# Performance work log

Measured on AMD Instinct MI355X. Metric: run time of the kernel, lower is better.

The kernel has to match this reference:

```python
import jax, jax.numpy as jnp
import numpy as np


def swiglu(g, u):
    return jax.nn.silu(g) * u


def setup_inputs() -> dict:
    key = jax.random.key(0)
    ks = jax.random.split(key, 10)
    D, H, E, HS = 2048, 512, 32, 1024
    B, S = 1, 2048
    s = 0.02
    return {
        "x": jax.random.normal(ks[0], (B, S, D), jnp.float32),
        "gate_w": jax.random.normal(ks[1], (E, D), jnp.float32) * s,
        "expert_bias": jnp.zeros((E,), jnp.float32),
        "wg": jax.random.normal(ks[2], (E, D, H), jnp.float32) * s,
        "wu": jax.random.normal(ks[3], (E, D, H), jnp.float32) * s,
        "wd": jax.random.normal(ks[4], (E, H, D), jnp.float32) * s,
        "sg": jax.random.normal(ks[5], (D, HS), jnp.float32) * s,
        "su": jax.random.normal(ks[6], (D, HS), jnp.float32) * s,
        "sd": jax.random.normal(ks[7], (HS, D), jnp.float32) * s,
        "coef_w": jax.random.normal(ks[8], (2, D), jnp.float32) * s,
        "coef_b": jnp.zeros((2,), jnp.float32),
        "top_k": 4,
    }


def reference(x, gate_w, expert_bias, wg, wu, wd, sg, su, sd, coef_w, coef_b, top_k):
    # --- sigmoid router with bias-adjusted top-k selection ---
    logits = jnp.einsum("bsd,ed->bse", x, gate_w)            # [B,S,E]
    routing = jax.nn.sigmoid(logits.astype(jnp.float32))
    biased = routing + expert_bias[None, None, :]
    _, inds = jax.lax.top_k(biased, top_k)                    # [B,S,k]
    scores = jnp.take_along_axis(routing, inds, axis=-1)      # gather UNbiased weights
    scores = scores / (jnp.sum(scores, axis=-1, keepdims=True) + 1e-20)  # norm_topk_prob
    scores = scores.astype(x.dtype)

    # --- SwitchGLU experts: dense per-expert SwiGLU, then gather top-k outputs ---
    h = jnp.einsum("bsd,edh->bseh", x, wg)                    # [B,S,E,H]
    u = jnp.einsum("bsd,edh->bseh", x, wu)
    y_all = jnp.einsum("bseh,ehd->bsed", swiglu(h, u), wd)    # [B,S,E,D]
    expert_out = jnp.take_along_axis(
        y_all, inds[..., None], axis=2)                        # [B,S,k,D]
    y_experts = jnp.sum(expert_out * scores[..., None], axis=-2)  # [B,S,D]

    # --- shared expert + learned 2-way mixing coefficient ---
    shared = swiglu(x @ sg, x @ su) @ sd                      # [B,S,D]
    coef = jax.nn.softmax(jnp.einsum("bsd,cd->bsc", x, coef_w) + coef_b, axis=-1)
    return y_experts * coef[..., :1] + shared * coef[..., 1:]
```

## Files before the change

### kernel.cpp

```cpp
#include <hip/hip_runtime.h>
#include <hip/hip_bf16.h>
#include <stdint.h>

#define S_TOK   2048
#define DMODEL  2048
#define HEXP    512
#define NEXP    32
#define HSH     1024
#define NPAIR   (S_TOK * 4)
#define NT128   96

#define M128_NT  0
#define M128_TE  1
#define M128_TP0 (1 + NT128)
#define M128_TM  (1 + 2 * NT128)
#define META_SIZE (1 + 3 * NT128)

typedef short  s16x8 __attribute__((ext_vector_type(8)));
typedef __bf16 b16x8 __attribute__((ext_vector_type(8)));
typedef float  f32x4 __attribute__((ext_vector_type(4)));

__device__ __forceinline__ f32x4 mfma16x16x32(s16x8 a, s16x8 b, f32x4 c) {
    return __builtin_amdgcn_mfma_f32_16x16x32_bf16(
        __builtin_bit_cast(b16x8, a), __builtin_bit_cast(b16x8, b), c, 0, 0, 0);
}

__device__ __forceinline__ unsigned short f2bf(float f) {
    union { float f; unsigned int u; } v; v.f = f;
    unsigned int u = v.u;
    return (unsigned short)((u + 0x7FFFu + ((u >> 16) & 1u)) >> 16);
}

__device__ __forceinline__ float bf2f(unsigned short b) {
    union { unsigned int u; float f; } v; v.u = ((unsigned int)b) << 16;
    return v.f;
}

__device__ __forceinline__ void gload16(const unsigned short* g, unsigned short* l) {
    __builtin_amdgcn_global_load_lds(
        (const __attribute__((address_space(1))) void*)(uintptr_t)g,
        (__attribute__((address_space(3))) void*)(uintptr_t)l, 16, 0, 0);
}

__device__ __forceinline__ int src_col8(int lane) {
    return 8 * ((lane & 3) ^ ((lane >> 3) & 3));
}
__device__ __forceinline__ int frag_ko(int fr, int fq) {
    return 8 * (fq ^ ((fr >> 1) & 3));
}

__device__ __forceinline__ void tconv_tile(const float* __restrict__ s,
                                           unsigned short* __restrict__ d,
                                           const int K, const int N,
                                           const int k0, const int n0,
                                           unsigned short* pool)
{
    auto T = (unsigned short (*)[84])pool;
    const int tid = threadIdx.x;
    const int n4 = (tid & 15) * 4;
    const int kr = tid >> 4;
#pragma unroll
    for (int i = 0; i < 4; ++i) {
        const int k = kr + i * 16;
        const float4 v = *reinterpret_cast<const float4*>(s + (size_t)(k0 + k) * N + n0 + n4);
        T[n4 + 0][k] = f2bf(v.x);
        T[n4 + 1][k] = f2bf(v.y);
        T[n4 + 2][k] = f2bf(v.z);
        T[n4 + 3][k] = f2bf(v.w);
    }
    __syncthreads();
    const int nw = tid >> 2;
    const int kc = (tid & 3) * 16;
    const uint2 a0 = *reinterpret_cast<const uint2*>(&T[nw][kc]);
    const uint2 a1 = *reinterpret_cast<const uint2*>(&T[nw][kc + 4]);
    const uint2 a2 = *reinterpret_cast<const uint2*>(&T[nw][kc + 8]);
    const uint2 a3 = *reinterpret_cast<const uint2*>(&T[nw][kc + 12]);
    uint4 w0, w1;
    w0.x = a0.x; w0.y = a0.y; w0.z = a1.x; w0.w = a1.y;
    w1.x = a2.x; w1.y = a2.y; w1.z = a3.x; w1.w = a3.y;
    unsigned short* o = d + (size_t)(n0 + nw) * K + k0 + kc;
    *reinterpret_cast<uint4*>(o)     = w0;
    *reinterpret_cast<uint4*>(o + 8) = w1;
}

__global__ __launch_bounds__(256)
void router_kernel(const float* __restrict__ x, const float* __restrict__ gate_w,
                   const float* __restrict__ expert_bias,
                   const float* __restrict__ coef_w, const float* __restrict__ coef_b,
                   int* __restrict__ inds, float* __restrict__ scores,
                   float* __restrict__ coefo)
{
    const int t = blockIdx.x;
    const int tid = threadIdx.x;
    const int lane = tid & 63;
    const int wave = tid >> 6;
    const float* xr = x + (size_t)t * DMODEL;

    float xv[32];
#pragma unroll
    for (int j = 0; j < 32; ++j) xv[j] = xr[lane + 64 * j];

    __shared__ float s_logits[NEXP];
    __shared__ float s_coef[2];

    for (int i = 0; i < 8; ++i) {
        const int e = wave * 8 + i;
        const float* wr = gate_w + (size_t)e * DMODEL;
        float p = 0.f;
#pragma unroll
        for (int j = 0; j < 32; ++j) p += xv[j] * wr[lane + 64 * j];
#pragma unroll
        for (int o = 32; o > 0; o >>= 1) p += __shfl_xor(p, o);
        if (lane == 0) s_logits[e] = p;
    }
    if (wave == 0) {
        for (int c = 0; c < 2; ++c) {
            const float* wr = coef_w + (size_t)c * DMODEL;
            float p = 0.f;
#pragma unroll
            for (int j = 0; j < 32; ++j) p += xv[j] * wr[lane + 64 * j];
#pragma unroll
            for (int o = 32; o > 0; o >>= 1) p += __shfl_xor(p, o);
            if (lane == 0) s_coef[c] = p;
        }
    }
    __syncthreads();
    if (tid == 0) {
        float routing[NEXP], biased[NEXP];
        for (int e = 0; e < NEXP; ++e) {
            const float r = 1.f / (1.f + expf(-s_logits[e]));
            routing[e] = r;
            biased[e] = r + expert_bias[e];
        }
        int sel[4]; float sc[4]; float ssum = 0.f;
        for (int k = 0; k < 4; ++k) {
            int best = 0; float bv = -1e30f;
            for (int e = 0; e < NEXP; ++e)
                if (biased[e] > bv) { bv = biased[e]; best = e; }
            sel[k] = best; sc[k] = routing[best]; ssum += sc[k];
            biased[best] = -1e30f;
        }
        const float inv = 1.f / (ssum + 1e-20f);
        for (int k = 0; k < 4; ++k) {
            inds[t * 4 + k] = sel[k];
            scores[t * 4 + k] = sc[k] * inv;
        }
        const float l0 = s_coef[0] + coef_b[0];
        const float l1 = s_coef[1] + coef_b[1];
        const float m = fmaxf(l0, l1);
        const float e0 = expf(l0 - m), e1 = expf(l1 - m);
        coefo[t * 2 + 0] = e0 / (e0 + e1);
        coefo[t * 2 + 1] = e1 / (e0 + e1);
    }
}

__global__ __launch_bounds__(256)
void xcast_kernel(const float* __restrict__ x, unsigned short* __restrict__ xb)
{
    const int i = (blockIdx.x * 256 + threadIdx.x) * 4;
    const float4 v = *reinterpret_cast<const float4*>(x + i);
    ushort4 o;
    o.x = f2bf(v.x); o.y = f2bf(v.y); o.z = f2bf(v.z); o.w = f2bf(v.w);
    *reinterpret_cast<ushort4*>(xb + i) = o;
}

__global__ __launch_bounds__(256)
void tconv_all_kernel(const float* __restrict__ wg, const float* __restrict__ wu,
                      const float* __restrict__ sg, const float* __restrict__ su,
                      unsigned short* __restrict__ W1, unsigned short* __restrict__ W2,
                      unsigned short* __restrict__ sgb, unsigned short* __restrict__ sub_)
{
    __shared__ unsigned short pool[64 * 84];
    const int bid = blockIdx.x;
    if (bid < 8192) {
        const int e = bid >> 8, t = bid & 255;
        tconv_tile(wg + (size_t)e * DMODEL * HEXP, W1 + (size_t)e * HEXP * DMODEL,
                   DMODEL, HEXP, ((t >> 3) & 31) * 64, (t & 7) * 64, pool);
    } else if (bid < 16384) {
        const int e = (bid - 8192) >> 8, t = bid & 255;
        tconv_tile(wu + (size_t)e * DMODEL * HEXP, W2 + (size_t)e * HEXP * DMODEL,
                   DMODEL, HEXP, ((t >> 3) & 31) * 64, (t & 7) * 64, pool);
    } else if (bid < 16896) {
        const int t = bid - 16384;
        tconv_tile(sg, sgb, DMODEL, HSH, (t >> 4) * 64, (t & 15) * 64, pool);
    } else {
        const int t = bid - 16896;
        tconv_tile(su, sub_, DMODEL, HSH, (t >> 4) * 64, (t & 15) * 64, pool);
    }
}

__global__ __launch_bounds__(1024)
void group_kernel(const int* __restrict__ inds, const float* __restrict__ scores,
                  int* __restrict__ meta, int* __restrict__ pair_token,
                  float* __restrict__ pair_score, int* __restrict__ tok_pos)
{
    __shared__ int cnt[NEXP];
    __shared__ int off_s[NEXP];
    __shared__ int cur[NEXP];
    const int tid = threadIdx.x;
    if (tid < NEXP) cnt[tid] = 0;
    __syncthreads();
    for (int i = tid; i < NPAIR; i += 1024) atomicAdd(&cnt[inds[i]], 1);
    __syncthreads();
    if (tid == 0) {
        int run = 0, nt1 = 0;
        for (int e = 0; e < NEXP; ++e) {
            off_s[e] = run;
            const int c = cnt[e];
            for (int m0 = 0; m0 < c; m0 += 128) {
                meta[M128_TE + nt1] = e;
                meta[M128_TP0 + nt1] = run + m0;
                meta[M128_TM + nt1] = (c - m0 < 128) ? (c - m0) : 128;
                ++nt1;
            }
            run += c;
        }
        meta[M128_NT] = nt1;
    }
    __syncthreads();
    if (tid < NEXP) cur[tid] = off_s[tid];
    __syncthreads();
    for (int i = tid; i < NPAIR; i += 1024) {
        const int e = inds[i];
        const int pos = atomicAdd(&cur[e], 1);
        pair_token[pos] = i >> 2;
        pair_score[pos] = scores[i];
        tok_pos[i] = pos;
    }
}

__global__ __launch_bounds__(256, 3)
void gu128_kernel(const unsigned short* __restrict__ xb,
                  const unsigned short* __restrict__ W1,
                  const unsigned short* __restrict__ W2,
                  const int* __restrict__ meta, const int* __restrict__ pair_token,
                  const unsigned short* __restrict__ sgb,
                  const unsigned short* __restrict__ sub_,
                  unsigned short* __restrict__ hexp, unsigned short* __restrict__ uexp,
                  unsigned short* __restrict__ shh, unsigned short* __restrict__ shu,
                  const float* __restrict__ wd, unsigned short* __restrict__ wdb,
                  const float* __restrict__ sd, unsigned short* __restrict__ sdb)
{
    constexpr int NT = DMODEL / 32;
    __shared__ unsigned short pool[16384];
    auto Al = (unsigned short (*)[128][32])(pool);
    auto Bl = (unsigned short (*)[128][32])(pool + 8192);

    const int bid = blockIdx.x;
    const int tid = threadIdx.x;
    const int lane = tid & 63;
    const int wave = tid >> 6;

    if (bid >= 8 * NT128 + 256) {
        const int idx = bid - (8 * NT128 + 256);
        if (idx < 8192) {
            const int e = idx >> 8, t = idx & 255;
            tconv_tile(wd + (size_t)e * HEXP * DMODEL, wdb + (size_t)e * DMODEL * HEXP,
                       HEXP, DMODEL, (t >> 5) * 64, (t & 31) * 64, pool);
        } else {
            const int t = idx - 8192;
            tconv_tile(sd, sdb, HSH, DMODEL, (t >> 5) * 64, (t & 31) * 64, pool);
        }
        return;
    }

    const int fr = lane & 15, fq = lane >> 4;
    const int ko = frag_ko(fr, fq);
    const int sub = lane >> 2;
    const int col8 = src_col8(lane);
    const int wm = wave >> 1, wn = wave & 1;
    const f32x4 zero4 = {0.f, 0.f, 0.f, 0.f};

    const bool EXPERT = bid < 8 * NT128;
    int p0, mval, n0, NB;
    const unsigned short* B;
    unsigned short* obuf;
    int tok0, tok1;
    const int arow0 = wave * 32 + sub;
    if (EXPERT) {
        const int tt = bid >> 3;
        if (tt >= meta[M128_NT]) return;
        const int e = meta[M128_TE + tt];
        p0 = meta[M128_TP0 + tt];
        mval = meta[M128_TM + tt];
        const int r = bid & 7;
        const int mat = r >> 2;
        n0 = (r & 3) * 128;
        NB = HEXP;
        B = (mat ? W2 : W1) + (size_t)e * HEXP * DMODEL;
        obuf = mat ? uexp : hexp;
        int q0 = p0 + arow0;      if (q0 > NPAIR - 1) q0 = NPAIR - 1;
        int q1 = p0 + arow0 + 16; if (q1 > NPAIR - 1) q1 = NPAIR - 1;
        tok0 = pair_token[q0];
        tok1 = pair_token[q1];
    } else {
        const int idx = bid - 8 * NT128;
        const int mat = idx & 1;
        n0 = ((idx >> 1) & 7) * 128;
        p0 = (idx >> 4) * 128;
        mval = 128;
        NB = HSH;
        B = mat ? sub_ : sgb;
        obuf = mat ? shu : shh;
        tok0 = p0 + arow0;
        tok1 = p0 + arow0 + 16;
    }

    const unsigned short* asrc0 = xb + (size_t)tok0 * DMODEL + col8;
    const unsigned short* asrc1 = xb + (size_t)tok1 * DMODEL + col8;
    const unsigned short* bsrc0 = B + (size_t)(n0 + arow0) * DMODEL + col8;
    const unsigned short* bsrc1 = B + (size_t)(n0 + arow0 + 16) * DMODEL + col8;

    auto stage = [&](int buf, int k0) {
        gload16(asrc0 + k0, &Al[buf][wave * 32][0]);
        gload16(asrc1 + k0, &Al[buf][wave * 32 + 16][0]);
        gload16(bsrc0 + k0, &Bl[buf][wave * 32][0]);
        gload16(bsrc1 + k0, &Bl[buf][wave * 32 + 16][0]);
    };

    f32x4 acc[4][4];
#pragma unroll
    for (int m = 0; m < 4; ++m)
#pragma unroll
        for (int n = 0; n < 4; ++n) acc[m][n] = zero4;

    auto compute = [&](int buf) {
        s16x8 af[4], bf[4];
#pragma unroll
        for (int m = 0; m < 4; ++m)
            af[m] = *reinterpret_cast<const s16x8*>(&Al[buf][wm * 64 + m * 16 + fr][ko]);
#pragma unroll
        for (int n = 0; n < 4; ++n)
            bf[n] = *reinterpret_cast<const s16x8*>(&Bl[buf][wn * 64 + n * 16 + fr][ko]);
#pragma unroll
        for (int m = 0; m < 4; ++m)
#pragma unroll
            for (int n = 0; n < 4; ++n)
                acc[m][n] = mfma16x16x32(af[m], bf[n], acc[m][n]);
    };

    stage(0, 0);
    __syncthreads();
#pragma unroll 1
    for (int t = 0; t < NT; ++t) {
        const int cur = t & 1;
        if (t + 1 < NT) stage(cur ^ 1, (t + 1) * 32);
        compute(cur);
        __syncthreads();
    }

#pragma unroll
    for (int m = 0; m < 4; ++m)
#pragma unroll
        for (int n = 0; n < 4; ++n) {
            const int col = n0 + wn * 64 + n * 16 + fr;
#pragma unroll
            for (int r = 0; r < 4; ++r) {
                const int rt = wm * 64 + m * 16 + fq * 4 + r;
                if (rt < mval)
                    obuf[(size_t)(p0 + rt) * NB + col] = f2bf(acc[m][n][r]);
            }
        }
}

__global__ __launch_bounds__(256)
void swiglu_kernel(const unsigned short* __restrict__ hexp,
                   const unsigned short* __restrict__ uexp,
                   unsigned short* __restrict__ act,
                   const unsigned short* __restrict__ shh,
                   const unsigned short* __restrict__ shu,
                   unsigned short* __restrict__ shact)
{
    constexpr size_t NE = (size_t)NPAIR * HEXP;
    const size_t i = ((size_t)blockIdx.x * 256 + threadIdx.x) * 8;
    const unsigned short *hp, *up;
    unsigned short* ap;
    size_t j;
    if (i < NE) { hp = hexp; up = uexp; ap = act; j = i; }
    else        { hp = shh;  up = shu;  ap = shact; j = i - NE; }
    const uint4 hv = *reinterpret_cast<const uint4*>(hp + j);
    const uint4 uv = *reinterpret_cast<const uint4*>(up + j);
    const unsigned short* hu = reinterpret_cast<const unsigned short*>(&hv);
    const unsigned short* uu = reinterpret_cast<const unsigned short*>(&uv);
    ushort4 o[2];
    unsigned short* ou = reinterpret_cast<unsigned short*>(o);
#pragma unroll
    for (int k = 0; k < 8; ++k) {
        const float h = bf2f(hu[k]);
        const float u = bf2f(uu[k]);
        ou[k] = f2bf(h / (1.f + __expf(-h)) * u);
    }
    *reinterpret_cast<uint4*>(ap + j) = *reinterpret_cast<const uint4*>(o);
}

__global__ __launch_bounds__(256, 3)
void down128_kernel(const unsigned short* __restrict__ act,
                    const unsigned short* __restrict__ shact,
                    const unsigned short* __restrict__ wdb,
                    const unsigned short* __restrict__ sdb,
                    unsigned short* __restrict__ ypair,
                    float* __restrict__ sdown,
                    const int* __restrict__ meta,
                    const float* __restrict__ pair_score)
{
    __shared__ unsigned short Al[2][128][32];
    __shared__ unsigned short Bl[2][128][32];

    const int bid = blockIdx.x;
    const int tid = threadIdx.x;
    const int lane = tid & 63;
    const int wave = tid >> 6;
    const int fr = lane & 15, fq = lane >> 4;
    const int ko = frag_ko(fr, fq);
    const int sub = lane >> 2;
    const int col8 = src_col8(lane);
    const int wm = wave >> 1, wn = wave & 1;
    const f32x4 zero4 = {0.f, 0.f, 0.f, 0.f};

    const bool EXPERT = bid < 16 * NT128;
    int p0, mval, n0, KA;
    const unsigned short *Asrc, *B;
    if (EXPERT) {
        const int tt = bid >> 4;
        if (tt >= meta[M128_NT]) return;
        const int e = meta[M128_TE + tt];
        p0 = meta[M128_TP0 + tt];
        mval = meta[M128_TM + tt];
        n0 = (bid & 15) * 128;
        KA = HEXP;
        Asrc = act;
        B = wdb + (size_t)e * DMODEL * HEXP;
    } else {
        const int idx = bid - 16 * NT128;
        p0 = (idx >> 4) * 128;
        mval = 128;
        n0 = (idx & 15) * 128;
        KA = HSH;
        Asrc = shact;
        B = sdb;
    }
    const int NT = KA / 32;

    const int arow0 = wave * 32 + sub;
    const unsigned short* asrc0 = Asrc + (size_t)(p0 + arow0) * KA + col8;
    const unsigned short* asrc1 = Asrc + (size_t)(p0 + arow0 + 16) * KA + col8;
    const unsigned short* bsrc0 = B + (size_t)(n0 + arow0) * KA + col8;
    const unsigned short* bsrc1 = B + (size_t)(n0 + arow0 + 16) * KA + col8;

    auto stage = [&](int buf, int k0) {
        gload16(asrc0 + k0, &Al[buf][wave * 32][0]);
        gload16(asrc1 + k0, &Al[buf][wave * 32 + 16][0]);
        gload16(bsrc0 + k0, &Bl[buf][wave * 32][0]);
        gload16(bsrc1 + k0, &Bl[buf][wave * 32 + 16][0]);
    };

    f32x4 acc[4][4];
#pragma unroll
    for (int m = 0; m < 4; ++m)
#pragma unroll
        for (int n = 0; n < 4; ++n) acc[m][n] = zero4;

    auto compute = [&](int buf) {
        s16x8 af[4], bf[4];
#pragma unroll
        for (int m = 0; m < 4; ++m)
            af[m] = *reinterpret_cast<const s16x8*>(&Al[buf][wm * 64 + m * 16 + fr][ko]);
#pragma unroll
        for (int n = 0; n < 4; ++n)
            bf[n] = *reinterpret_cast<const s16x8*>(&Bl[buf][wn * 64 + n * 16 + fr][ko]);
#pragma unroll
        for (int m = 0; m < 4; ++m)
#pragma unroll
            for (int n = 0; n < 4; ++n)
                acc[m][n] = mfma16x16x32(af[m], bf[n], acc[m][n]);
    };

    stage(0, 0);
    __syncthreads();
#pragma unroll 1
    for (int t = 0; t < NT; ++t) {
        const int cur = t & 1;
        if (t + 1 < NT) stage(cur ^ 1, (t + 1) * 32);
        compute(cur);
        __syncthreads();
    }

#pragma unroll
    for (int m = 0; m < 4; ++m)
#pragma unroll
        for (int n = 0; n < 4; ++n) {
            const int col = n0 + wn * 64 + n * 16 + fr;
#pragma unroll
            for (int r = 0; r < 4; ++r) {
                const int rt = wm * 64 + m * 16 + fq * 4 + r;
                if (rt < mval) {
                    if (EXPERT) {
                        const int p = p0 + rt;
                        ypair[(size_t)p * DMODEL + col] = f2bf(acc[m][n][r] * pair_score[p]);
                    } else {
                        sdown[(size_t)(p0 + rt) * DMODEL + col] = acc[m][n][r];
                    }
                }
            }
        }
}

__global__ __launch_bounds__(256)
void final_kernel(const unsigned short* __restrict__ ypair,
                  const float* __restrict__ sdown,
                  const float* __restrict__ coef, const int* __restrict__ tok_pos,
                  float* __restrict__ out)
{
    const int row = blockIdx.x;
    const int col = threadIdx.x * 8;
    float acc[8] = {0.f, 0.f, 0.f, 0.f, 0.f, 0.f, 0.f, 0.f};
#pragma unroll
    for (int k = 0; k < 4; ++k) {
        const int pos = tok_pos[row * 4 + k];
        const uint4 v = *reinterpret_cast<const uint4*>(ypair + (size_t)pos * DMODEL + col);
        const unsigned short* u = reinterpret_cast<const unsigned short*>(&v);
#pragma unroll
        for (int j = 0; j < 8; ++j) acc[j] += bf2f(u[j]);
    }
    const float c0 = coef[row * 2 + 0];
    const float c1 = coef[row * 2 + 1];
    const float* sd = sdown + (size_t)row * DMODEL + col;
    const float4 s0 = *reinterpret_cast<const float4*>(sd);
    const float4 s1 = *reinterpret_cast<const float4*>(sd + 4);
    float4 o0, o1;
    o0.x = acc[0] * c0 + s0.x * c1; o0.y = acc[1] * c0 + s0.y * c1;
    o0.z = acc[2] * c0 + s0.z * c1; o0.w = acc[3] * c0 + s0.w * c1;
    o1.x = acc[4] * c0 + s1.x * c1; o1.y = acc[5] * c0 + s1.y * c1;
    o1.z = acc[6] * c0 + s1.z * c1; o1.w = acc[7] * c0 + s1.w * c1;
    float* op = out + (size_t)row * DMODEL + col;
    *reinterpret_cast<float4*>(op) = o0;
    *reinterpret_cast<float4*>(op + 4) = o1;
}

extern "C" void kernel_launch(void* const* d_in, const int* in_sizes, int n_in,
                              void* d_out, int out_size, void* d_ws, size_t ws_size,
                              hipStream_t stream)
{
    const float* x           = (const float*)d_in[0];
    const float* gate_w      = (const float*)d_in[1];
    const float* expert_bias = (const float*)d_in[2];
    const float* wg          = (const float*)d_in[3];
    const float* wu          = (const float*)d_in[4];
    const float* wd          = (const float*)d_in[5];
    const float* sg          = (const float*)d_in[6];
    const float* su          = (const float*)d_in[7];
    const float* sd          = (const float*)d_in[8];
    const float* coef_w      = (const float*)d_in[9];
    const float* coef_b      = (const float*)d_in[10];
    float* out = (float*)d_out;

    char* ws = (char*)d_ws;
    size_t off = 0;
    auto take = [&](size_t bytes) {
        char* p = ws + off;
        off = (off + bytes + 255) & ~(size_t)255;
        return p;
    };
    int*   inds     = (int*)  take((size_t)S_TOK * 4 * sizeof(int));
    float* scores   = (float*)take((size_t)S_TOK * 4 * sizeof(float));
    float* coefp    = (float*)take((size_t)S_TOK * 2 * sizeof(float));
    int*   meta     = (int*)  take((size_t)META_SIZE * sizeof(int));
    int*   pair_tok = (int*)  take((size_t)NPAIR * sizeof(int));
    float* pair_sc  = (float*)take((size_t)NPAIR * sizeof(float));
    int*   tok_pos  = (int*)  take((size_t)NPAIR * sizeof(int));
    unsigned short* xb    = (unsigned short*)take((size_t)S_TOK * DMODEL * 2);
    unsigned short* act   = (unsigned short*)take((size_t)NPAIR * HEXP * 2);
    unsigned short* hexp  = (unsigned short*)take((size_t)NPAIR * HEXP * 2);
    unsigned short* uexp  = (unsigned short*)take((size_t)NPAIR * HEXP * 2);
    unsigned short* shact = (unsigned short*)take((size_t)S_TOK * HSH * 2);
    unsigned short* shh   = (unsigned short*)take((size_t)S_TOK * HSH * 2);
    unsigned short* shu   = (unsigned short*)take((size_t)S_TOK * HSH * 2);
    unsigned short* ypair = (unsigned short*)take((size_t)NPAIR * DMODEL * 2);
    float*          sdown = (float*)take((size_t)S_TOK * DMODEL * 4);
    unsigned short* sgb   = (unsigned short*)take((size_t)HSH * DMODEL * 2);
    unsigned short* sub_  = (unsigned short*)take((size_t)HSH * DMODEL * 2);
    unsigned short* sdb   = (unsigned short*)take((size_t)DMODEL * HSH * 2);
    unsigned short* W1    = (unsigned short*)take((size_t)NEXP * DMODEL * HEXP * 2);
    unsigned short* W2    = (unsigned short*)take((size_t)NEXP * DMODEL * HEXP * 2);
    unsigned short* wdb   = (unsigned short*)take((size_t)NEXP * DMODEL * HEXP * 2);
    (void)ws_size; (void)in_sizes; (void)n_in; (void)out_size;

    router_kernel<<<S_TOK, 256, 0, stream>>>(x, gate_w, expert_bias, coef_w, coef_b,
                                             inds, scores, coefp);
    xcast_kernel<<<(S_TOK * DMODEL / 4) / 256, 256, 0, stream>>>(x, xb);
    group_kernel<<<1, 1024, 0, stream>>>(inds, scores, meta, pair_tok, pair_sc, tok_pos);

    tconv_all_kernel<<<17408, 256, 0, stream>>>(wg, wu, sg, su, W1, W2, sgb, sub_);

    gu128_kernel<<<8 * NT128 + 256 + 8704, 256, 0, stream>>>(
        xb, W1, W2, meta, pair_tok, sgb, sub_, hexp, uexp, shh, shu,
        wd, wdb, sd, sdb);

    swiglu_kernel<<<3072, 256, 0, stream>>>(hexp, uexp, act, shh, shu, shact);

    down128_kernel<<<16 * NT128 + 256, 256, 0, stream>>>(
        act, shact, wdb, sdb, ypair, sdown, meta, pair_sc);

    final_kernel<<<S_TOK, 256, 0, stream>>>(ypair, sdown, coefp, tok_pos, out);
}
```

Before: 333.6 us.

## Swizzle block IDs across XCDs, XOR-swizzle transpose LDS, fold xcast into tconv

Adds a `swz8` block-index remap to the weight-transpose, gate/up and down kernels. On this GPU consecutive blocks are dealt round-robin across the 8 XCDs, so the remap groups neighbouring logical tiles onto the same XCD to improve L2 reuse. The transpose tile's LDS buffer drops its padded 84-wide rows for 64-wide rows with an XOR swizzle, which lets each thread read its output with two 16-byte loads instead of four 8-byte loads. The separate x-to-bf16 cast kernel is folded into the transpose kernel as extra blocks, removing one launch. The risks are a different tail-block distribution and that the swizzle only stays correct while the grid sizes remain multiples of 8.

```diff
diff --git a/kernel.cpp b/kernel.cpp
--- a/kernel.cpp
+++ b/kernel.cpp
@@ -49,35 +49,37 @@
     return 8 * (fq ^ ((fr >> 1) & 3));
 }
 
+__device__ __forceinline__ int swz8(int bid, int n) {
+    return (bid & 7) * (n >> 3) + (bid >> 3);
+}
+
 __device__ __forceinline__ void tconv_tile(const float* __restrict__ s,
                                            unsigned short* __restrict__ d,
                                            const int K, const int N,
                                            const int k0, const int n0,
                                            unsigned short* pool)
 {
-    auto T = (unsigned short (*)[84])pool;
+    auto T = (unsigned short (*)[64])pool;
     const int tid = threadIdx.x;
     const int n4 = (tid & 15) * 4;
     const int kr = tid >> 4;
+    const int wkey = ((n4 >> 2) & 7) << 3;
 #pragma unroll
     for (int i = 0; i < 4; ++i) {
         const int k = kr + i * 16;
         const float4 v = *reinterpret_cast<const float4*>(s + (size_t)(k0 + k) * N + n0 + n4);
-        T[n4 + 0][k] = f2bf(v.x);
-        T[n4 + 1][k] = f2bf(v.y);
-        T[n4 + 2][k] = f2bf(v.z);
-        T[n4 + 3][k] = f2bf(v.w);
+        const int kk = k ^ wkey;
+        T[n4 + 0][kk] = f2bf(v.x);
+        T[n4 + 1][kk] = f2bf(v.y);
+        T[n4 + 2][kk] = f2bf(v.z);
+        T[n4 + 3][kk] = f2bf(v.w);
     }
     __syncthreads();
     const int nw = tid >> 2;
     const int kc = (tid & 3) * 16;
-    const uint2 a0 = *reinterpret_cast<const uint2*>(&T[nw][kc]);
-    const uint2 a1 = *reinterpret_cast<const uint2*>(&T[nw][kc + 4]);
-    const uint2 a2 = *reinterpret_cast<const uint2*>(&T[nw][kc + 8]);
-    const uint2 a3 = *reinterpret_cast<const uint2*>(&T[nw][kc + 12]);
-    uint4 w0, w1;
-    w0.x = a0.x; w0.y = a0.y; w0.z = a1.x; w0.w = a1.y;
-    w1.x = a2.x; w1.y = a2.y; w1.z = a3.x; w1.w = a3.y;
+    const int rkey = ((nw >> 2) & 7) << 3;
+    const uint4 w0 = *reinterpret_cast<const uint4*>(&T[nw][kc ^ rkey]);
+    const uint4 w1 = *reinterpret_cast<const uint4*>(&T[nw][(kc + 8) ^ rkey]);
     unsigned short* o = d + (size_t)(n0 + nw) * K + k0 + kc;
     *reinterpret_cast<uint4*>(o)     = w0;
     *reinterpret_cast<uint4*>(o + 8) = w1;
@@ -155,23 +157,14 @@
 }
 
 __global__ __launch_bounds__(256)
-void xcast_kernel(const float* __restrict__ x, unsigned short* __restrict__ xb)
-{
-    const int i = (blockIdx.x * 256 + threadIdx.x) * 4;
-    const float4 v = *reinterpret_cast<const float4*>(x + i);
-    ushort4 o;
-    o.x = f2bf(v.x); o.y = f2bf(v.y); o.z = f2bf(v.z); o.w = f2bf(v.w);
-    *reinterpret_cast<ushort4*>(xb + i) = o;
-}
-
-__global__ __launch_bounds__(256)
 void tconv_all_kernel(const float* __restrict__ wg, const float* __restrict__ wu,
                       const float* __restrict__ sg, const float* __restrict__ su,
                       unsigned short* __restrict__ W1, unsigned short* __restrict__ W2,
-                      unsigned short* __restrict__ sgb, unsigned short* __restrict__ sub_)
-{
-    __shared__ unsigned short pool[64 * 84];
-    const int bid = blockIdx.x;
+                      unsigned short* __restrict__ sgb, unsigned short* __restrict__ sub_,
+                      const float* __restrict__ x, unsigned short* __restrict__ xb)
+{
+    __shared__ unsigned short pool[64 * 64];
+    const int bid = swz8(blockIdx.x, 21504);
     if (bid < 8192) {
         const int e = bid >> 8, t = bid & 255;
         tconv_tile(wg + (size_t)e * DMODEL * HEXP, W1 + (size_t)e * HEXP * DMODEL,
@@ -183,9 +176,16 @@
     } else if (bid < 16896) {
         const int t = bid - 16384;
         tconv_tile(sg, sgb, DMODEL, HSH, (t >> 4) * 64, (t & 15) * 64, pool);
-    } else {
+    } else if (bid < 17408) {
         const int t = bid - 16896;
         tconv_tile(su, sub_, DMODEL, HSH, (t >> 4) * 64, (t & 15) * 64, pool);
+    } else {
+        const int idx = bid - 17408;
+        const int i = (idx * 256 + (int)threadIdx.x) * 4;
+        const float4 v = *reinterpret_cast<const float4*>(x + i);
+        ushort4 o;
+        o.x = f2bf(v.x); o.y = f2bf(v.y); o.z = f2bf(v.z); o.w = f2bf(v.w);
+        *reinterpret_cast<ushort4*>(xb + i) = o;
     }
 }
 
@@ -246,7 +246,7 @@
     auto Al = (unsigned short (*)[128][32])(pool);
     auto Bl = (unsigned short (*)[128][32])(pool + 8192);
 
-    const int bid = blockIdx.x;
+    const int bid = swz8(blockIdx.x, 8 * NT128 + 256 + 8704);
     const int tid = threadIdx.x;
     const int lane = tid & 63;
     const int wave = tid >> 6;
@@ -406,7 +406,7 @@
     __shared__ unsigned short Al[2][128][32];
     __shared__ unsigned short Bl[2][128][32];
 
-    const int bid = blockIdx.x;
+    const int bid = swz8(blockIdx.x, 16 * NT128 + 256);
     const int tid = threadIdx.x;
     const int lane = tid & 63;
     const int wave = tid >> 6;
@@ -587,10 +587,9 @@
 
     router_kernel<<<S_TOK, 256, 0, stream>>>(x, gate_w, expert_bias, coef_w, coef_b,
                                              inds, scores, coefp);
-    xcast_kernel<<<(S_TOK * DMODEL / 4) / 256, 256, 0, stream>>>(x, xb);
     group_kernel<<<1, 1024, 0, stream>>>(inds, scores, meta, pair_tok, pair_sc, tok_pos);
 
-    tconv_all_kernel<<<17408, 256, 0, stream>>>(wg, wu, sg, su, W1, W2, sgb, sub_);
+    tconv_all_kernel<<<21504, 256, 0, stream>>>(wg, wu, sg, su, W1, W2, sgb, sub_, x, xb);
 
     gu128_kernel<<<8 * NT128 + 256 + 8704, 256, 0, stream>>>(
         xb, W1, W2, meta, pair_tok, sgb, sub_, hexp, uexp, shh, shu,
```

Result: slower. 820.3 us (+145.9%).
